# Performance work log

Measured on AMD Instinct MI355X. Metric: run time of the kernel, lower is better.

Reference implementation:

```python
import jax, jax.numpy as jnp
import numpy as np
from jax import lax

B, H, W, C = 4, 1024, 1024, 16


def setup_inputs() -> dict:
    key = jax.random.key(0)
    k1, k2 = jax.random.split(key)
    feat = jax.random.normal(k1, (B, H, W, C), dtype=jnp.float32)
    mask = jax.random.randint(k2, (B, H, W), 0, 2).astype(bool)
    return {"feat": feat, "mask": mask}


def _sum_pool(f, m):
    """Minkowski sum pooling, kernel 3, stride 2, dilation 1, dim 2.

    Output coord c exists iff any input coord in {2c, 2c+1}^2 is occupied
    (floor(coord/2) strided coordinate map). Output feature at c sums input
    features at 2c + {-1,0,1}^2 (3x3 window centered on the strided coord).
    """
    f = f * m[..., None].astype(f.dtype)  # zero features at empty coords
    # 3x3 sum window, stride 2, pad 1 -> output spatial dims H//2, W//2
    out = lax.reduce_window(
        f, jnp.zeros((), f.dtype), lax.add,
        window_dimensions=(1, 3, 3, 1),
        window_strides=(1, 2, 2, 1),
        padding=((0, 0), (1, 1), (1, 1), (0, 0)),
    )
    b, h, w = m.shape
    m2 = m.reshape(b, h // 2, 2, w // 2, 2).any(axis=(2, 4))  # strided coord map
    out = out * m2[..., None].astype(out.dtype)  # keep only occupied outputs
    return out, m2


def reference(feat, mask):
    c1, m1 = _sum_pool(feat, mask)
    c2, m2 = _sum_pool(c1, m1)
    c3, m3 = _sum_pool(c2, m2)
    return (c2, c3)
```

## Files before the change

kernel.cpp:

```cpp
#include <hip/hip_runtime.h>


constexpr int Hh = 1024, Ww = 1024;
constexpr int TW3 = 16, TH3 = 8;
constexpr int NU = 4 * TW3 + 3;
constexpr int NV = 2 * TW3 + 1;
constexpr int NY = TW3;
constexpr int NTH = 320;
constexpr int NS = 4 * TH3 + 3;

#define BARRIER_LDS() asm volatile("s_waitcnt lgkmcnt(0)\ns_barrier" ::: "memory")

__device__ inline float4 add3(const float4& a, const float4& b, const float4& c) {
    return make_float4(a.x + b.x + c.x, a.y + b.y + c.y,
                       a.z + b.z + c.z, a.w + b.w + c.w);
}

__global__ __launch_bounds__(NTH) void fused3(
    const float* __restrict__ featp, const int* __restrict__ maskp,
    float4* __restrict__ c2o, float4* __restrict__ c3o)
{
    const int j = blockIdx.x;
    const int k = blockIdx.y;
    const int b = blockIdx.z;
    const int P0 = TW3 * j, Q0 = TH3 * k;
    const int F0 = 8 * P0 - 7;
    const int S0 = 4 * Q0 - 3;

    const int tid = threadIdx.x;
    const int c4 = tid & 3;
    const int u  = tid >> 2;
    const bool aAct = tid < NU * 4;
    const bool vAct = tid < NV * 4;
    const bool yAct = tid < NY * 4;

    __shared__ float4 c1m[2][NU][5];
    __shared__ float4 c2mS[NV][5];
    __shared__ unsigned char m1L[2][NU];
    __shared__ unsigned char m2L[NV];

    const float4* feat4 = reinterpret_cast<const float4*>(featp);
    const float4 z4 = make_float4(0.f, 0.f, 0.f, 0.f);

    auto ldMaskRow = [&](int t, int* mm) {
        mm[0] = mm[1] = mm[2] = 0;
        if (aAct && (unsigned)t < (unsigned)Hh) {
            const int base = (b * Hh + t) * Ww;
#pragma unroll
            for (int dw = 0; dw < 3; ++dw) {
                const int fc = F0 + 2 * u + dw;
                if ((unsigned)fc < (unsigned)Ww) mm[dw] = maskp[base + fc];
            }
        }
    };
    auto ldFeatRow = [&](int t, const int* mm, float4* ff) {
        ff[0] = ff[1] = ff[2] = z4;
        if (aAct && (unsigned)t < (unsigned)Hh) {
            const size_t base = (size_t)(b * Hh + t) * Ww;
#pragma unroll
            for (int dw = 0; dw < 3; ++dw) {
                if (mm[dw])
                    ff[dw] = feat4[(base + (F0 + 2 * u + dw)) * 4 + c4];
            }
        }
    };

    int   mA[6];
    float4 ffA[6];
    float4 h_prev;
    int   mp_cur;
    {
        int mP[3], m0[6];
        ldMaskRow(2 * S0 - 1, mP);
        ldMaskRow(2 * S0,     m0);
        ldMaskRow(2 * S0 + 1, m0 + 3);
        ldMaskRow(2 * S0 + 2, mA);
        ldMaskRow(2 * S0 + 3, mA + 3);
        float4 fP[3];
        ldFeatRow(2 * S0 - 1, mP, fP);
        ldFeatRow(2 * S0,     m0, ffA);
        ldFeatRow(2 * S0 + 1, m0 + 3, ffA + 3);
        h_prev = add3(fP[0], fP[1], fP[2]);
        mp_cur = m0[1] | m0[2] | m0[4] | m0[5];
    }

    float4 r2h0 = z4, r2h1 = z4;
    float4 r3h0 = z4, r3h1 = z4;
    int m2save = 0, m3save = 0;

    for (int i = 0; i < NS; ++i) {
        const int sb = i & 1;
        const float4 hc_e = add3(ffA[0], ffA[1], ffA[2]);
        const float4 hc_o = add3(ffA[3], ffA[4], ffA[5]);
        if (aAct) {
            float4 cv = z4;
            if (mp_cur) cv = add3(h_prev, hc_e, hc_o);
            c1m[sb][u][c4] = cv;
            if (c4 == 0) m1L[sb][u] = (unsigned char)(mp_cur ? 1 : 0);
        }
        const float4 hp_new = hc_o;
        const int mp_new = mA[1] | mA[2] | mA[4] | mA[5];
        const int t2 = 2 * (S0 + i) + 2;
        if (i + 1 < NS) {
            ldFeatRow(t2,     mA,     ffA);
            ldFeatRow(t2 + 1, mA + 3, ffA + 3);
        }
        if (i + 2 < NS) {
            ldMaskRow(t2 + 2, mA);
            ldMaskRow(t2 + 3, mA + 3);
        }
        BARRIER_LDS();
        float4 r2c = z4; int m2p = 0;
        if (vAct) {
            r2c = add3(c1m[sb][2 * u + 0][c4], c1m[sb][2 * u + 1][c4],
                       c1m[sb][2 * u + 2][c4]);
            m2p = m1L[sb][2 * u + 1] | m1L[sb][2 * u + 2];
        }
        if ((i & 1) == 0) {
            if (vAct) {
                const int m2 = m2save | m2p;
                float4 c2v = z4;
                if (m2) c2v = add3(r2h0, r2h1, r2c);
                if (i >= 4 && u >= 1) {
                    const int r = 2 * Q0 - 2 + (i >> 1);
                    c2o[((size_t)((b * 256 + r) * 256 + (2 * P0 - 1 + u))) * 4 + c4] = c2v;
                }
                c2mS[u][c4] = c2v;
                if (c4 == 0) m2L[u] = (unsigned char)(m2 ? 1 : 0);
            }
        } else {
            m2save = m2p;
            float4 r3c = z4; int m3p = 0;
            if (yAct) {
                r3c = add3(c2mS[2 * u + 0][c4], c2mS[2 * u + 1][c4],
                           c2mS[2 * u + 2][c4]);
                m3p = m2L[2 * u + 1] | m2L[2 * u + 2];
            }
            if (((i - 1) & 2) == 0) {
                m3save = m3p;
            } else if (yAct && i >= 7) {
                const int m3 = m3save | m3p;
                float4 c3v = z4;
                if (m3) c3v = add3(r3h0, r3h1, r3c);
                const int q = Q0 + ((i - 7) >> 2);
                c3o[((size_t)((b * 128 + q) * 128 + (P0 + u))) * 4 + c4] = c3v;
            }
            r3h0 = r3h1; r3h1 = r3c;
        }
        r2h0 = r2h1; r2h1 = r2c;
        h_prev = hp_new; mp_cur = mp_new;
    }
    BARRIER_LDS();
    if (yAct) {
        const float4 r3c = add3(c2mS[2 * u + 0][c4], c2mS[2 * u + 1][c4],
                                c2mS[2 * u + 2][c4]);
        const int m3p = m2L[2 * u + 1] | m2L[2 * u + 2];
        const int m3 = m3save | m3p;
        float4 c3v = z4;
        if (m3) c3v = add3(r3h0, r3h1, r3c);
        const int q = Q0 + ((NS - 7) >> 2);
        c3o[((size_t)((b * 128 + q) * 128 + (P0 + u))) * 4 + c4] = c3v;
    }
}

extern "C" void kernel_launch(void* const* d_in, const int* in_sizes, int n_in,
                              void* d_out, int out_size, void* d_ws, size_t ws_size,
                              hipStream_t stream)
{
    const float* feat = (const float*)d_in[0];
    const int*   mask = (const int*)d_in[1];
    float4* c2 = (float4*)d_out;
    float4* c3 = c2 + (size_t)4 * 256 * 256 * 4;

    dim3 grid(Ww / (8 * TW3) , Hh / (8 * TH3) , 4);
    fused3<<<grid, NTH, 0, stream>>>(feat, mask, c2, c3);
}
```

Before: 60.48 us.

## Prefetch feature rows two steps ahead with rotating double-buffered registers

Deepens the software pipeline: feature row pairs are loaded two iterations ahead into alternating register buffers, and mask rows four iterations ahead using three rotating mask buffers. The loop is unrolled by six so the buffer rotation resolves at compile time. The final c3 epilogue is folded into one extra loop iteration. This aims to hide more global-memory latency per wave, at the cost of extra VGPRs that could reduce occupancy.

```diff
diff --git a/kernel.cpp b/kernel.cpp
--- a/kernel.cpp
+++ b/kernel.cpp
@@ -8,6 +8,7 @@
 constexpr int NY = TW3;
 constexpr int NTH = 320;
 constexpr int NS = 4 * TH3 + 3;
+constexpr int NITER = NS + 1;
 
 #define BARRIER_LDS() asm volatile("s_waitcnt lgkmcnt(0)\ns_barrier" ::: "memory")
 
@@ -64,51 +65,55 @@
             }
         }
     };
+    auto ldMaskPair = [&](int p, int* m6) {
+        ldMaskRow(2 * (S0 + p),     m6);
+        ldMaskRow(2 * (S0 + p) + 1, m6 + 3);
+    };
+    auto ldFeatPair = [&](int p, const int* m6, float4* f6) {
+        ldFeatRow(2 * (S0 + p),     m6,     f6);
+        ldFeatRow(2 * (S0 + p) + 1, m6 + 3, f6 + 3);
+    };
+    auto occ = [&](const int* m6) { return m6[1] | m6[2] | m6[4] | m6[5]; };
 
-    int   mA[6];
-    float4 ffA[6];
+    int M0[6], M1[6], M2[6];
+    float4 ffA[6], ffB[6];
     float4 h_prev;
-    int   mp_cur;
+    int mpA, mpB;
     {
-        int mP[3], m0[6];
+        int mP[3];
         ldMaskRow(2 * S0 - 1, mP);
-        ldMaskRow(2 * S0,     m0);
-        ldMaskRow(2 * S0 + 1, m0 + 3);
-        ldMaskRow(2 * S0 + 2, mA);
-        ldMaskRow(2 * S0 + 3, mA + 3);
+        ldMaskPair(0, M0);
+        ldMaskPair(1, M1);
+        ldMaskPair(2, M2);
         float4 fP[3];
         ldFeatRow(2 * S0 - 1, mP, fP);
-        ldFeatRow(2 * S0,     m0, ffA);
-        ldFeatRow(2 * S0 + 1, m0 + 3, ffA + 3);
+        ldFeatPair(0, M0, ffA);
+        ldFeatPair(1, M1, ffB);
+        mpA = occ(M0);
+        mpB = occ(M1);
+        ldMaskPair(3, M0);
         h_prev = add3(fP[0], fP[1], fP[2]);
-        mp_cur = m0[1] | m0[2] | m0[4] | m0[5];
     }
 
     float4 r2h0 = z4, r2h1 = z4;
     float4 r3h0 = z4, r3h1 = z4;
     int m2save = 0, m3save = 0;
 
-    for (int i = 0; i < NS; ++i) {
+    auto body = [&](int i, float4 (&FF)[6], int (&MG)[6], int (&MN)[6]) {
         const int sb = i & 1;
-        const float4 hc_e = add3(ffA[0], ffA[1], ffA[2]);
-        const float4 hc_o = add3(ffA[3], ffA[4], ffA[5]);
+        const float4 hc_e = add3(FF[0], FF[1], FF[2]);
+        const float4 hc_o = add3(FF[3], FF[4], FF[5]);
         if (aAct) {
             float4 cv = z4;
-            if (mp_cur) cv = add3(h_prev, hc_e, hc_o);
+            if (mpA) cv = add3(h_prev, hc_e, hc_o);
             c1m[sb][u][c4] = cv;
-            if (c4 == 0) m1L[sb][u] = (unsigned char)(mp_cur ? 1 : 0);
+            if (c4 == 0) m1L[sb][u] = (unsigned char)(mpA ? 1 : 0);
         }
-        const float4 hp_new = hc_o;
-        const int mp_new = mA[1] | mA[2] | mA[4] | mA[5];
-        const int t2 = 2 * (S0 + i) + 2;
-        if (i + 1 < NS) {
-            ldFeatRow(t2,     mA,     ffA);
-            ldFeatRow(t2 + 1, mA + 3, ffA + 3);
-        }
-        if (i + 2 < NS) {
-            ldMaskRow(t2 + 2, mA);
-            ldMaskRow(t2 + 3, mA + 3);
-        }
+        h_prev = hc_o;
+        mpA = mpB;
+        mpB = occ(MG);
+        if (i + 2 < NS) ldFeatPair(i + 2, MG, FF);
+        if (i + 4 < NS) ldMaskPair(i + 4, MN);
         BARRIER_LDS();
         float4 r2c = z4; int m2p = 0;
         if (vAct) {
@@ -148,18 +153,15 @@
             r3h0 = r3h1; r3h1 = r3c;
         }
         r2h0 = r2h1; r2h1 = r2c;
-        h_prev = hp_new; mp_cur = mp_new;
-    }
-    BARRIER_LDS();
-    if (yAct) {
-        const float4 r3c = add3(c2mS[2 * u + 0][c4], c2mS[2 * u + 1][c4],
-                                c2mS[2 * u + 2][c4]);
-        const int m3p = m2L[2 * u + 1] | m2L[2 * u + 2];
-        const int m3 = m3save | m3p;
-        float4 c3v = z4;
-        if (m3) c3v = add3(r3h0, r3h1, r3c);
-        const int q = Q0 + ((NS - 7) >> 2);
-        c3o[((size_t)((b * 128 + q) * 128 + (P0 + u))) * 4 + c4] = c3v;
+    };
+
+    for (int ii = 0; ii < NITER; ii += 6) {
+        body(ii + 0, ffA, M2, M1);
+        body(ii + 1, ffB, M0, M2);
+        body(ii + 2, ffA, M1, M0);
+        body(ii + 3, ffB, M2, M1);
+        body(ii + 4, ffA, M0, M2);
+        body(ii + 5, ffB, M1, M0);
     }
 }
 
```

New measurement: 99.27 us. 64.2% more time.
